# Optimization experiments

Hardware: AMD Instinct MI355X
Metric: run time of the kernel (lower is better)

Reference implementation:

```python
import jax, jax.numpy as jnp
import numpy as np

NUM_WORDS = 35000
EMBED_DIM = 100
MAX_LEN = 80
BATCH = 2048
UNITS = 512


def setup_inputs() -> dict:
    key = jax.random.key(0)
    ks = jax.random.split(key, 7)
    inputs = jax.random.randint(ks[0], (BATCH, MAX_LEN), 0, NUM_WORDS)
    emb_table = jax.random.normal(ks[1], (NUM_WORDS, EMBED_DIM), jnp.float32) * 0.05
    W_xh = jax.random.normal(ks[2], (EMBED_DIM, UNITS), jnp.float32) * (1.0 / np.sqrt(EMBED_DIM))
    W_hh = jax.random.normal(ks[3], (UNITS, UNITS), jnp.float32) * (1.0 / np.sqrt(UNITS))
    b_h = jnp.zeros((UNITS,), jnp.float32)
    W_out = jax.random.normal(ks[4], (UNITS, 1), jnp.float32) * (1.0 / np.sqrt(UNITS))
    b_out = jnp.zeros((1,), jnp.float32)
    return {"inputs": inputs, "emb_table": emb_table, "W_xh": W_xh,
            "W_hh": W_hh, "b_h": b_h, "W_out": W_out, "b_out": b_out}


def reference(inputs, emb_table, W_xh, W_hh, b_h, W_out, b_out):
    # Embedding lookup: [B, T, D]
    x = emb_table[inputs]
    # Precompute input projection for all timesteps (batched GEMM): [B, T, U]
    xw = jnp.einsum('btd,du->btu', x, W_xh) + b_h
    h0 = jnp.zeros((inputs.shape[0], W_hh.shape[0]), x.dtype)

    def step(h, xt):
        # SimpleRNNCell (inference, dropout off): h' = tanh(x@W_xh + b + h@W_hh)
        h_new = jnp.tanh(xt + h @ W_hh)
        return h_new, None

    # scan over time axis; carry only the [B, U] hidden state
    h_last, _ = jax.lax.scan(step, h0, jnp.swapaxes(xw, 0, 1))
    logits = h_last @ W_out + b_out  # [B, 1]
    return jax.nn.sigmoid(logits)
```

## Files before the change

kernel.cpp:

```cpp
#include <hip/hip_runtime.h>
#include <hip/hip_bf16.h>


#define T_LEN   80
#define EMB_D   100
#define UNITS   512
#define ROWS    16
#define NBLK    128
#define NTHR    512
#define NT      4
#define KSH     16
#define KSX     4
#define KSALL   (KSX + KSH)
#define SDEPTH  3

typedef __bf16 bf16x8 __attribute__((ext_vector_type(8)));
typedef float  f32x4  __attribute__((ext_vector_type(4)));

__device__ __forceinline__ float fast_tanh(float x) {
    float e = __builtin_amdgcn_exp2f(x * 2.8853900817779268f);
    return 1.0f - 2.0f * __builtin_amdgcn_rcpf(1.0f + e);
}

__global__ void prep_kernel(const float* __restrict__ Whh,
                            const float* __restrict__ Wxh,
                            __bf16* __restrict__ Wt, __bf16* __restrict__ Xt) {
    __shared__ float tile[32][33];
    const int tx = threadIdx.x & 31, ty = threadIdx.x >> 5;
    const int b = blockIdx.x;
    if (b < 256) {
        const int k0 = (b & 15) * 32, n0 = (b >> 4) * 32;
        #pragma unroll
        for (int i = 0; i < 4; ++i)
            tile[ty + 8 * i][tx] = Whh[(k0 + ty + 8 * i) * UNITS + n0 + tx];
        __syncthreads();
        #pragma unroll
        for (int i = 0; i < 4; ++i) {
            const int n = ty + 8 * i;
            Wt[(n0 + n) * UNITS + k0 + tx] = (__bf16)tile[tx][n];
        }
    } else {
        const int bb = b - 256;
        const int k0 = (bb & 3) * 32, n0 = (bb >> 2) * 32;
        #pragma unroll
        for (int i = 0; i < 4; ++i) {
            const int k = k0 + ty + 8 * i;
            tile[ty + 8 * i][tx] = (k < EMB_D) ? Wxh[k * UNITS + n0 + tx] : 0.0f;
        }
        __syncthreads();
        #pragma unroll
        for (int i = 0; i < 4; ++i) {
            const int n = ty + 8 * i;
            Xt[(n0 + n) * 128 + k0 + tx] = (__bf16)tile[tx][n];
        }
    }
}

__global__ __launch_bounds__(NTHR)
__attribute__((amdgpu_waves_per_eu(2, 2)))
void rnn_kernel(const int*   __restrict__ inputs,
                const float* __restrict__ emb,
                const float* __restrict__ bh,
                const float* __restrict__ Wout,
                const float* __restrict__ bout,
                const __bf16* __restrict__ Wt,
                const __bf16* __restrict__ Xt,
                float*       __restrict__ out)
{
    __shared__ alignas(16) __bf16 hbuf[2][ROWS * UNITS];
    __shared__ alignas(16) __bf16 xbuf[2][ROWS * 128];

    const int tid  = threadIdx.x;
    const int wave = tid >> 6;
    const int lane = tid & 63;
    const int q    = lane >> 4;
    const int ln   = lane & 15;
    const int e7   = ln & 7;
    const int qa   = q ^ (e7 & 3);
    const int kx   = e7 >> 2;
    const int q8   = q << 3;
    const int r0   = blockIdx.x * ROWS;

    int   woff[NT], xoff[NT];
    float bhv[NT];
    #pragma unroll
    for (int nt = 0; nt < NT; ++nt) {
        const int col = (wave << 6) + (nt << 4) + ln;
        woff[nt] = col * UNITS + q8;
        xoff[nt] = col * 128   + q8;
        bhv[nt]  = bh[col];
    }

    {
        int4 z; z.x = z.y = z.z = z.w = 0;
        int4* hp = (int4*)&hbuf[0][0];
        #pragma unroll
        for (int i = 0; i < 4; ++i) hp[tid + i * NTHR] = z;
        int4* xp = (int4*)&xbuf[0][0];
        xp[tid] = z;
    }
    __syncthreads();

    auto stage = [&](int t, __bf16* xb) {
        #pragma unroll
        for (int rr = 0; rr < 2; ++rr) {
            const int r = wave + (rr << 3);
            const int idxv = inputs[(r0 + r) * T_LEN + t];
            const float* er = emb + (size_t)idxv * EMB_D;
            const int k0 = lane;
            xb[(r << 7) + ((((k0 >> 3) ^ (r & 7)) << 3) | (k0 & 7))] = (__bf16)er[k0];
            const int k1 = lane + 64;
            if (k1 < EMB_D)
                xb[(r << 7) + ((((k1 >> 3) ^ (r & 7)) << 3) | (k1 & 7))] = (__bf16)er[k1];
        }
    };

    auto step = [&](const __bf16* hb_r, const __bf16* xb_r, __bf16* hb_w) {
        bf16x8 sB[SDEPTH][NT];
        #pragma unroll
        for (int p = 0; p < SDEPTH; ++p)
            #pragma unroll
            for (int nt = 0; nt < NT; ++nt)
                sB[p][nt] = (p < KSX)
                    ? *(const bf16x8*)(Xt + xoff[nt] + (p << 5))
                    : *(const bf16x8*)(Wt + woff[nt] + ((p - KSX) << 5));

        f32x4 acc[NT];
        #pragma unroll
        for (int nt = 0; nt < NT; ++nt) {
            f32x4 a = {bhv[nt], bhv[nt], bhv[nt], bhv[nt]};
            acc[nt] = a;
        }

        const int xb0 = (ln << 7) + (qa << 3);
        const int hb0 = (ln << 9) + (qa << 3);
        #pragma unroll
        for (int i = 0; i < KSALL; ++i) {
            const int s = i % SDEPTH;
            bf16x8 a;
            if (i < KSX)
                a = *(const bf16x8*)&xb_r[xb0 + ((i ^ kx) << 5)];
            else
                a = *(const bf16x8*)&hb_r[hb0 + (((i - KSX) ^ kx) << 5)];
            #pragma unroll
            for (int nt = 0; nt < NT; ++nt)
                acc[nt] = __builtin_amdgcn_mfma_f32_16x16x32_bf16(a, sB[s][nt], acc[nt], 0, 0, 0);
            if (i + SDEPTH < KSALL) {
                const int j = i + SDEPTH;
                #pragma unroll
                for (int nt = 0; nt < NT; ++nt)
                    sB[s][nt] = (j < KSX)
                        ? *(const bf16x8*)(Xt + xoff[nt] + (j << 5))
                        : *(const bf16x8*)(Wt + woff[nt] + ((j - KSX) << 5));
            }
        }
        #pragma unroll
        for (int nt = 0; nt < NT; ++nt) {
            const int cc = (wave << 3) + (nt << 1) + (ln >> 3);
            #pragma unroll
            for (int i = 0; i < 4; ++i) {
                const int row = (q << 2) + i;
                hb_w[(row << 9) + (((cc ^ (row & 7)) << 3) | (ln & 7))] =
                    (__bf16)fast_tanh(acc[nt][i]);
            }
        }
    };

    stage(0, xbuf[0]);
    __syncthreads();

    #pragma unroll 1
    for (int t = 0; t < T_LEN; t += 2) {
        stage(t + 1, xbuf[1]);
        step(hbuf[0], xbuf[0], hbuf[1]);
        __syncthreads();
        if (t + 2 < T_LEN) stage(t + 2, xbuf[0]);
        step(hbuf[1], xbuf[1], hbuf[0]);
        __syncthreads();
    }

    #pragma unroll
    for (int rr = 0; rr < 2; ++rr) {
        const int m = wave + (rr << 3);
        const bf16x8 hv = *(const bf16x8*)&hbuf[0][(m << 9) + ((lane ^ (m & 7)) << 3)];
        float s = 0.0f;
        #pragma unroll
        for (int j = 0; j < 8; ++j)
            s += (float)hv[j] * Wout[(lane << 3) + j];
        #pragma unroll
        for (int off = 32; off > 0; off >>= 1)
            s += __shfl_down(s, off, 64);
        if (lane == 0) {
            const float logit = s + bout[0];
            out[r0 + m] = __builtin_amdgcn_rcpf(
                1.0f + __builtin_amdgcn_exp2f(-logit * 1.4426950408889634f));
        }
    }
}

extern "C" void kernel_launch(void* const* d_in, const int* in_sizes, int n_in,
                              void* d_out, int out_size, void* d_ws, size_t ws_size,
                              hipStream_t stream) {
    __bf16* Wt = (__bf16*)d_ws;
    __bf16* Xt = Wt + UNITS * UNITS;
    prep_kernel<<<dim3(320), dim3(256), 0, stream>>>(
        (const float*)d_in[3],
        (const float*)d_in[2],
        Wt, Xt);
    rnn_kernel<<<dim3(NBLK), dim3(NTHR), 0, stream>>>(
        (const int*)d_in[0],
        (const float*)d_in[1],
        (const float*)d_in[4],
        (const float*)d_in[5],
        (const float*)d_in[6],
        Wt, Xt,
        (float*)d_out);
}
```

Measured before the change: 1.336 ms.

## Process 32 rows per block and pre-swizzle weights into MFMA fragment order

Each block now handles 32 batch rows using two M-tiles, so every weight fragment loaded from global/L2 feeds twice as many MFMAs, and only 64 blocks are launched. The prep kernel writes W_xh and W_hh into a fragment-ordered layout, so each lane's per-step weight load is a contiguous 16-byte read from a per-wave slice. This halves weight traffic per row, but uses only 64 of the device's CUs and doubles LDS and accumulator register use per block.

Measured after the change: 1.647 ms. 1.23x slower.

```diff
diff --git a/kernel.cpp b/kernel.cpp
--- a/kernel.cpp
+++ b/kernel.cpp
@@ -5,14 +5,16 @@
 #define T_LEN   80
 #define EMB_D   100
 #define UNITS   512
-#define ROWS    16
-#define NBLK    128
+#define ROWS    32
+#define NBLK    64
 #define NTHR    512
+#define NW      8
 #define NT      4
+#define KSX     4
 #define KSH     16
-#define KSX     4
 #define KSALL   (KSX + KSH)
 #define SDEPTH  3
+#define WSLICE  (KSALL * NT * 64 * 8)
 
 typedef __bf16 bf16x8 __attribute__((ext_vector_type(8)));
 typedef float  f32x4  __attribute__((ext_vector_type(4)));
@@ -24,36 +26,30 @@
 
 __global__ void prep_kernel(const float* __restrict__ Whh,
                             const float* __restrict__ Wxh,
-                            __bf16* __restrict__ Wt, __bf16* __restrict__ Xt) {
-    __shared__ float tile[32][33];
-    const int tx = threadIdx.x & 31, ty = threadIdx.x >> 5;
-    const int b = blockIdx.x;
-    if (b < 256) {
-        const int k0 = (b & 15) * 32, n0 = (b >> 4) * 32;
-        #pragma unroll
-        for (int i = 0; i < 4; ++i)
-            tile[ty + 8 * i][tx] = Whh[(k0 + ty + 8 * i) * UNITS + n0 + tx];
-        __syncthreads();
-        #pragma unroll
-        for (int i = 0; i < 4; ++i) {
-            const int n = ty + 8 * i;
-            Wt[(n0 + n) * UNITS + k0 + tx] = (__bf16)tile[tx][n];
-        }
+                            __bf16* __restrict__ Wf) {
+    const int f    = blockIdx.x * 256 + threadIdx.x;
+    const int lane = f & 63;
+    const int t2   = f >> 6;
+    const int nt   = t2 & (NT - 1);
+    const int t3   = t2 >> 2;
+    const int i    = t3 % KSALL;
+    const int wave = t3 / KSALL;
+    const int col  = (wave << 6) + (nt << 4) + (lane & 15);
+    const int q    = lane >> 4;
+    bf16x8 v;
+    if (i < KSX) {
+        const int k0 = (i << 5) + (q << 3);
+        #pragma unroll
+        for (int j = 0; j < 8; ++j)
+            v[j] = (k0 + j < EMB_D) ? (__bf16)Wxh[(k0 + j) * UNITS + col]
+                                    : (__bf16)0.0f;
     } else {
-        const int bb = b - 256;
-        const int k0 = (bb & 3) * 32, n0 = (bb >> 2) * 32;
-        #pragma unroll
-        for (int i = 0; i < 4; ++i) {
-            const int k = k0 + ty + 8 * i;
-            tile[ty + 8 * i][tx] = (k < EMB_D) ? Wxh[k * UNITS + n0 + tx] : 0.0f;
-        }
-        __syncthreads();
-        #pragma unroll
-        for (int i = 0; i < 4; ++i) {
-            const int n = ty + 8 * i;
-            Xt[(n0 + n) * 128 + k0 + tx] = (__bf16)tile[tx][n];
-        }
-    }
+        const int k0 = ((i - KSX) << 5) + (q << 3);
+        #pragma unroll
+        for (int j = 0; j < 8; ++j)
+            v[j] = (__bf16)Whh[(k0 + j) * UNITS + col];
+    }
+    *(bf16x8*)(Wf + (size_t)f * 8) = v;
 }
 
 __global__ __launch_bounds__(NTHR)
@@ -63,8 +59,7 @@
                 const float* __restrict__ bh,
                 const float* __restrict__ Wout,
                 const float* __restrict__ bout,
-                const __bf16* __restrict__ Wt,
-                const __bf16* __restrict__ Xt,
+                const __bf16* __restrict__ Wf,
                 float*       __restrict__ out)
 {
     __shared__ alignas(16) __bf16 hbuf[2][ROWS * UNITS];
@@ -78,33 +73,30 @@
     const int e7   = ln & 7;
     const int qa   = q ^ (e7 & 3);
     const int kx   = e7 >> 2;
-    const int q8   = q << 3;
     const int r0   = blockIdx.x * ROWS;
 
-    int   woff[NT], xoff[NT];
+    const __bf16* wbase = Wf + (size_t)wave * WSLICE + (lane << 3);
+
     float bhv[NT];
     #pragma unroll
-    for (int nt = 0; nt < NT; ++nt) {
-        const int col = (wave << 6) + (nt << 4) + ln;
-        woff[nt] = col * UNITS + q8;
-        xoff[nt] = col * 128   + q8;
-        bhv[nt]  = bh[col];
-    }
+    for (int nt = 0; nt < NT; ++nt)
+        bhv[nt] = bh[(wave << 6) + (nt << 4) + ln];
 
     {
         int4 z; z.x = z.y = z.z = z.w = 0;
         int4* hp = (int4*)&hbuf[0][0];
         #pragma unroll
-        for (int i = 0; i < 4; ++i) hp[tid + i * NTHR] = z;
+        for (int i = 0; i < 8; ++i) hp[tid + i * NTHR] = z;
         int4* xp = (int4*)&xbuf[0][0];
-        xp[tid] = z;
+        #pragma unroll
+        for (int i = 0; i < 2; ++i) xp[tid + i * NTHR] = z;
     }
     __syncthreads();
 
     auto stage = [&](int t, __bf16* xb) {
         #pragma unroll
-        for (int rr = 0; rr < 2; ++rr) {
-            const int r = wave + (rr << 3);
+        for (int rr = 0; rr < 4; ++rr) {
+            const int r = (wave << 2) + rr;
             const int idxv = inputs[(r0 + r) * T_LEN + t];
             const float* er = emb + (size_t)idxv * EMB_D;
             const int k0 = lane;
@@ -121,49 +113,55 @@
         for (int p = 0; p < SDEPTH; ++p)
             #pragma unroll
             for (int nt = 0; nt < NT; ++nt)
-                sB[p][nt] = (p < KSX)
-                    ? *(const bf16x8*)(Xt + xoff[nt] + (p << 5))
-                    : *(const bf16x8*)(Wt + woff[nt] + ((p - KSX) << 5));
-
-        f32x4 acc[NT];
-        #pragma unroll
-        for (int nt = 0; nt < NT; ++nt) {
-            f32x4 a = {bhv[nt], bhv[nt], bhv[nt], bhv[nt]};
-            acc[nt] = a;
-        }
+                sB[p][nt] = *(const bf16x8*)(wbase + (((p * NT + nt)) << 9));
+
+        f32x4 acc[2][NT];
+        #pragma unroll
+        for (int mt = 0; mt < 2; ++mt)
+            #pragma unroll
+            for (int nt = 0; nt < NT; ++nt) {
+                f32x4 a = {bhv[nt], bhv[nt], bhv[nt], bhv[nt]};
+                acc[mt][nt] = a;
+            }
 
         const int xb0 = (ln << 7) + (qa << 3);
         const int hb0 = (ln << 9) + (qa << 3);
         #pragma unroll
         for (int i = 0; i < KSALL; ++i) {
             const int s = i % SDEPTH;
-            bf16x8 a;
-            if (i < KSX)
-                a = *(const bf16x8*)&xb_r[xb0 + ((i ^ kx) << 5)];
-            else
-                a = *(const bf16x8*)&hb_r[hb0 + (((i - KSX) ^ kx) << 5)];
+            bf16x8 a0, a1;
+            if (i < KSX) {
+                a0 = *(const bf16x8*)&xb_r[xb0 + ((i ^ kx) << 5)];
+                a1 = *(const bf16x8*)&xb_r[xb0 + (16 << 7) + ((i ^ kx) << 5)];
+            } else {
+                a0 = *(const bf16x8*)&hb_r[hb0 + (((i - KSX) ^ kx) << 5)];
+                a1 = *(const bf16x8*)&hb_r[hb0 + (16 << 9) + (((i - KSX) ^ kx) << 5)];
+            }
             #pragma unroll
             for (int nt = 0; nt < NT; ++nt)
-                acc[nt] = __builtin_amdgcn_mfma_f32_16x16x32_bf16(a, sB[s][nt], acc[nt], 0, 0, 0);
+                acc[0][nt] = __builtin_amdgcn_mfma_f32_16x16x32_bf16(a0, sB[s][nt], acc[0][nt], 0, 0, 0);
+            #pragma unroll
+            for (int nt = 0; nt < NT; ++nt)
+                acc[1][nt] = __builtin_amdgcn_mfma_f32_16x16x32_bf16(a1, sB[s][nt], acc[1][nt], 0, 0, 0);
             if (i + SDEPTH < KSALL) {
                 const int j = i + SDEPTH;
                 #pragma unroll
                 for (int nt = 0; nt < NT; ++nt)
-                    sB[s][nt] = (j < KSX)
-                        ? *(const bf16x8*)(Xt + xoff[nt] + (j << 5))
-                        : *(const bf16x8*)(Wt + woff[nt] + ((j - KSX) << 5));
+                    sB[s][nt] = *(const bf16x8*)(wbase + ((j * NT + nt) << 9));
             }
         }
         #pragma unroll
-        for (int nt = 0; nt < NT; ++nt) {
-            const int cc = (wave << 3) + (nt << 1) + (ln >> 3);
-            #pragma unroll
-            for (int i = 0; i < 4; ++i) {
-                const int row = (q << 2) + i;
-                hb_w[(row << 9) + (((cc ^ (row & 7)) << 3) | (ln & 7))] =
-                    (__bf16)fast_tanh(acc[nt][i]);
-            }
-        }
+        for (int mt = 0; mt < 2; ++mt)
+            #pragma unroll
+            for (int nt = 0; nt < NT; ++nt) {
+                const int cc = (wave << 3) + (nt << 1) + (ln >> 3);
+                #pragma unroll
+                for (int i = 0; i < 4; ++i) {
+                    const int row = (mt << 4) + (q << 2) + i;
+                    hb_w[(row << 9) + (((cc ^ (row & 7)) << 3) | (ln & 7))] =
+                        (__bf16)fast_tanh(acc[mt][nt][i]);
+                }
+            }
     };
 
     stage(0, xbuf[0]);
@@ -180,8 +178,8 @@
     }
 
     #pragma unroll
-    for (int rr = 0; rr < 2; ++rr) {
-        const int m = wave + (rr << 3);
+    for (int rr = 0; rr < 4; ++rr) {
+        const int m = (wave << 2) + rr;
         const bf16x8 hv = *(const bf16x8*)&hbuf[0][(m << 9) + ((lane ^ (m & 7)) << 3)];
         float s = 0.0f;
         #pragma unroll
@@ -201,18 +199,17 @@
 extern "C" void kernel_launch(void* const* d_in, const int* in_sizes, int n_in,
                               void* d_out, int out_size, void* d_ws, size_t ws_size,
                               hipStream_t stream) {
-    __bf16* Wt = (__bf16*)d_ws;
-    __bf16* Xt = Wt + UNITS * UNITS;
-    prep_kernel<<<dim3(320), dim3(256), 0, stream>>>(
+    __bf16* Wf = (__bf16*)d_ws;
+    prep_kernel<<<dim3(160), dim3(256), 0, stream>>>(
         (const float*)d_in[3],
         (const float*)d_in[2],
-        Wt, Xt);
+        Wf);
     rnn_kernel<<<dim3(NBLK), dim3(NTHR), 0, stream>>>(
         (const int*)d_in[0],
         (const float*)d_in[1],
         (const float*)d_in[4],
         (const float*)d_in[5],
         (const float*)d_in[6],
-        Wt, Xt,
+        Wf,
         (float*)d_out);
 }
```
